# Kernel tuning notes

Hardware: AMD Instinct MI355X
Metric: run time of the kernel (lower is better)

The kernel has to match this reference:

```python
import jax, jax.numpy as jnp
import numpy as np

EMBED = 768
HEADS = 12
HEAD_DIM = EMBED // HEADS
B, S = 2, 2048


def setup_inputs() -> dict:
    key = jax.random.key(0)
    ks = jax.random.split(key, 5)
    scale = 1.0 / np.sqrt(EMBED)
    return {
        "x": jax.random.normal(ks[0], (B, S, EMBED), dtype=jnp.float32),
        "w_q": jax.random.normal(ks[1], (EMBED, EMBED), dtype=jnp.float32) * scale,
        "b_q": jnp.zeros((EMBED,), dtype=jnp.float32),
        "w_k": jax.random.normal(ks[2], (EMBED, EMBED), dtype=jnp.float32) * scale,
        "b_k": jnp.zeros((EMBED,), dtype=jnp.float32),
        "w_v": jax.random.normal(ks[3], (EMBED, EMBED), dtype=jnp.float32) * scale,
        "b_v": jnp.zeros((EMBED,), dtype=jnp.float32),
        "w_o": jax.random.normal(ks[4], (EMBED, EMBED), dtype=jnp.float32) * scale,
        "b_o": jnp.zeros((EMBED,), dtype=jnp.float32),
    }


def reference(x, w_q, b_q, w_k, b_k, w_v, b_v, w_o, b_o):
    b, s, _ = x.shape
    # QKV projections (torch Linear: y = x @ W^T + b)
    q = x @ w_q.T + b_q
    k = x @ w_k.T + b_k
    v = x @ w_v.T + b_v
    # split heads -> [b, h, s, d]
    def split(t):
        return t.reshape(b, s, HEADS, HEAD_DIM).transpose(0, 2, 1, 3)
    q, k, v = split(q), split(k), split(v)
    scores = jnp.einsum("bhqd,bhkd->bhqk", q, k) / jnp.sqrt(
        jnp.asarray(HEAD_DIM, dtype=jnp.float32))
    probs = jax.nn.softmax(scores, axis=-1)
    out = jnp.einsum("bhqk,bhkd->bhqd", probs, v)
    out = out.transpose(0, 2, 1, 3).reshape(b, s, EMBED)
    return out @ w_o.T + b_o
```

## Files before the change

### kernel.cpp

```cpp
#include <hip/hip_runtime.h>
#include <math.h>

#define EMBED 768
#define HEADS 12
#define HDIM 64
#define BATCH 2
#define SEQ 2048
#define MTOT (BATCH*SEQ)

typedef short s8v __attribute__((ext_vector_type(8)));
typedef short s4v __attribute__((ext_vector_type(4)));
typedef float f4v __attribute__((ext_vector_type(4)));

__device__ __forceinline__ short f2bf(float f) {
    union { float f; unsigned u; } v; v.f = f;
    unsigned r = v.u + 0x7FFFu + ((v.u >> 16) & 1u);
    return (short)(r >> 16);
}

__device__ __forceinline__ unsigned pkbf(float a, float b) {
#if __has_builtin(__builtin_amdgcn_cvt_pk_bf16_f32)
    typedef __bf16 b2 __attribute__((ext_vector_type(2)));
    b2 r = __builtin_amdgcn_cvt_pk_bf16_f32(a, b);
    return *(unsigned*)&r;
#else
    union { float f; unsigned u; } x, y; x.f = a; y.f = b;
    return ((y.u + 0x8000u) & 0xFFFF0000u) | ((x.u + 0x8000u) >> 16);
#endif
}

__device__ __forceinline__ float fexp2(float x) {
#if __has_builtin(__builtin_amdgcn_exp2f)
    return __builtin_amdgcn_exp2f(x);
#else
    return exp2f(x);
#endif
}

__device__ __forceinline__ void gll16(const short* g, short* l) {
    __builtin_amdgcn_global_load_lds((const __attribute__((address_space(1))) void*)g,
                                     (__attribute__((address_space(3))) void*)l, 16, 0, 0);
}

__global__ __launch_bounds__(256) void cvt_all(
        const float* __restrict__ x,  const float* __restrict__ wq,
        const float* __restrict__ wk, const float* __restrict__ wv,
        const float* __restrict__ wo,
        short* __restrict__ xb, short* __restrict__ wqb, short* __restrict__ wkb,
        short* __restrict__ wvb, short* __restrict__ wob) {
    const int seg = blockIdx.y;
    const float* src; short* dst; int n4;
    if      (seg == 0) { src = x;  dst = xb;  n4 = MTOT * EMBED / 4; }
    else if (seg == 1) { src = wq; dst = wqb; n4 = EMBED * EMBED / 4; }
    else if (seg == 2) { src = wk; dst = wkb; n4 = EMBED * EMBED / 4; }
    else if (seg == 3) { src = wv; dst = wvb; n4 = EMBED * EMBED / 4; }
    else               { src = wo; dst = wob; n4 = EMBED * EMBED / 4; }
    for (int i = blockIdx.x * 256 + threadIdx.x; i < n4; i += gridDim.x * 256) {
        float4 f = ((const float4*)src)[i];
        short4 o;
        o.x = f2bf(f.x); o.y = f2bf(f.y); o.z = f2bf(f.z); o.w = f2bf(f.w);
        ((short4*)dst)[i] = o;
    }
}

__global__ __launch_bounds__(256, 4) void gemm_qkv(const short* __restrict__ A,
        const short* __restrict__ Wq, const short* __restrict__ Wk, const short* __restrict__ Wv,
        const float* __restrict__ bq, const float* __restrict__ bk, const float* __restrict__ bv,
        short* __restrict__ Qo, short* __restrict__ Ko, short* __restrict__ Vo) {
    const int mode = blockIdx.z;
    const short* W    = (mode == 0) ? Wq : (mode == 1) ? Wk : Wv;
    const float* bias = (mode == 0) ? bq : (mode == 1) ? bk : bv;

    __shared__ short smem[12288];
    short* As0 = smem;        short* As1 = smem + 2048;
    short* Ws0 = smem + 4096; short* Ws1 = smem + 8192;

    const int tid = threadIdx.x;
    const int lane = tid & 63, wid = tid >> 6;
    const int quad = lane >> 4, lr = lane & 15;
    const int m0 = blockIdx.x * 64, n0 = blockIdx.y * 128;
    const int wm = (wid >> 1) * 32, wn = (wid & 1) * 64;
    const int ar = lane >> 2, ac = (lane & 3) * 8;

    f4v acc[2][4];
    for (int a = 0; a < 2; a++)
        for (int b = 0; b < 4; b++)
            for (int i = 0; i < 4; i++) acc[a][b][i] = 0.f;

    const short* gA  = &A[(long)(m0 + wid * 16 + ar) * EMBED + ac];
    const short* gW0 = &W[(long)(n0 + wid * 32 + ar) * EMBED + ac];
    const short* gW1 = &W[(long)(n0 + wid * 32 + 16 + ar) * EMBED + ac];
    short* dA  = smem + wid * 512;
    short* dW0 = smem + 4096 + wid * 1024;
    short* dW1 = dW0 + 512;

    gll16(gA, dA); gll16(gW0, dW0); gll16(gW1, dW1);
    gA += 32; gW0 += 32; gW1 += 32;
    __syncthreads();

    for (int k = 0; k < 24; k += 2) {
        gll16(gA, dA + 2048); gll16(gW0, dW0 + 4096); gll16(gW1, dW1 + 4096);
        gA += 32; gW0 += 32; gW1 += 32;
        {
            s8v af[2], bf[4];
            for (int mi = 0; mi < 2; mi++)
                af[mi] = *(const s8v*)&As0[(wm + mi * 16 + lr) * 32 + quad * 8];
            for (int ni = 0; ni < 4; ni++)
                bf[ni] = *(const s8v*)&Ws0[(wn + ni * 16 + lr) * 32 + quad * 8];
            for (int mi = 0; mi < 2; mi++)
                for (int ni = 0; ni < 4; ni++)
                    acc[mi][ni] = __builtin_amdgcn_mfma_f32_16x16x32_bf16(af[mi], bf[ni], acc[mi][ni], 0, 0, 0);
        }
        __syncthreads();
        if (k + 2 < 24) {
            gll16(gA, dA); gll16(gW0, dW0); gll16(gW1, dW1);
            gA += 32; gW0 += 32; gW1 += 32;
        }
        {
            s8v af[2], bf[4];
            for (int mi = 0; mi < 2; mi++)
                af[mi] = *(const s8v*)&As1[(wm + mi * 16 + lr) * 32 + quad * 8];
            for (int ni = 0; ni < 4; ni++)
                bf[ni] = *(const s8v*)&Ws1[(wn + ni * 16 + lr) * 32 + quad * 8];
            for (int mi = 0; mi < 2; mi++)
                for (int ni = 0; ni < 4; ni++)
                    acc[mi][ni] = __builtin_amdgcn_mfma_f32_16x16x32_bf16(af[mi], bf[ni], acc[mi][ni], 0, 0, 0);
        }
        __syncthreads();
    }

    float bb[4];
    for (int ni = 0; ni < 4; ni++) bb[ni] = bias[n0 + wn + ni * 16 + lr];

    if (mode == 2) {
        for (int mi = 0; mi < 2; mi++) {
            int srow = m0 + wm + mi * 16 + quad * 4;
            int b = srow >> 11, s = srow & 2047;
            int v = s & 127, r = s >> 7;
            int keyp = r * 128 + (((v >> 5) * 4 + ((v >> 2) & 3)) << 3) + ((v >> 4) & 1) * 4;
            for (int ni = 0; ni < 4; ni++) {
                int n = n0 + wn + ni * 16 + lr;
                int h = n >> 6, d = n & 63;
                uint2 pk;
                pk.x = pkbf(acc[mi][ni][0] + bb[ni], acc[mi][ni][1] + bb[ni]);
                pk.y = pkbf(acc[mi][ni][2] + bb[ni], acc[mi][ni][3] + bb[ni]);
                *(uint2*)&Vo[(((long)(b * HEADS + h) * HDIM + d) * SEQ) + keyp] = pk;
            }
        }
    } else {
        const float qsc = (mode == 0) ? 0.18033688f : 1.0f;
        short* Cs = smem;
        for (int mi = 0; mi < 2; mi++)
            for (int ni = 0; ni < 4; ni++)
                for (int i = 0; i < 4; i++)
                    Cs[(wm + mi * 16 + quad * 4 + i) * 136 + wn + ni * 16 + lr] =
                        f2bf((acc[mi][ni][i] + bb[ni]) * qsc);
        __syncthreads();
        short* Out = (mode == 0) ? Qo : Ko;
        int r = tid >> 2, seg = tid & 3;
        int m = m0 + r, b = m >> 11, s = m & 2047;
        int nn = seg * 32;
        int h = (n0 + nn) >> 6, d = nn & 63;
        short* dst = &Out[(((long)(b * HEADS + h) * SEQ + s) * HDIM) + d];
        const short* src = &Cs[r * 136 + nn];
        for (int j = 0; j < 4; j++)
            *(s8v*)(dst + j * 8) = *(const s8v*)(src + j * 8);
    }
}

__global__ __launch_bounds__(256, 4) void gemm_out(const short* __restrict__ A,
        const short* __restrict__ W, const float* __restrict__ bias,
        float* __restrict__ Out) {
    __shared__ short smem[8192];
    short* As0 = smem;        short* As1 = smem + 2048;
    short* Ws0 = smem + 4096; short* Ws1 = smem + 6144;

    const int tid = threadIdx.x;
    const int lane = tid & 63, wid = tid >> 6;
    const int quad = lane >> 4, lr = lane & 15;
    const int m0 = blockIdx.x * 64, n0 = blockIdx.y * 64;
    const int wm = (wid >> 1) * 32, wn = (wid & 1) * 32;
    const int ar = lane >> 2, ac = (lane & 3) * 8;

    f4v acc[2][2];
    for (int a = 0; a < 2; a++)
        for (int b = 0; b < 2; b++)
            for (int i = 0; i < 4; i++) acc[a][b][i] = 0.f;

    const short* gA = &A[(long)(m0 + wid * 16 + ar) * EMBED + ac];
    const short* gW = &W[(long)(n0 + wid * 16 + ar) * EMBED + ac];
    short* dA = smem + wid * 512;
    short* dW = smem + 4096 + wid * 512;

    gll16(gA, dA); gll16(gW, dW);
    gA += 32; gW += 32;
    __syncthreads();

    for (int k = 0; k < 24; k += 2) {
        gll16(gA, dA + 2048); gll16(gW, dW + 2048);
        gA += 32; gW += 32;
        {
            s8v af[2], bf[2];
            for (int mi = 0; mi < 2; mi++)
                af[mi] = *(const s8v*)&As0[(wm + mi * 16 + lr) * 32 + quad * 8];
            for (int ni = 0; ni < 2; ni++)
                bf[ni] = *(const s8v*)&Ws0[(wn + ni * 16 + lr) * 32 + quad * 8];
            for (int mi = 0; mi < 2; mi++)
                for (int ni = 0; ni < 2; ni++)
                    acc[mi][ni] = __builtin_amdgcn_mfma_f32_16x16x32_bf16(af[mi], bf[ni], acc[mi][ni], 0, 0, 0);
        }
        __syncthreads();
        if (k + 2 < 24) {
            gll16(gA, dA); gll16(gW, dW);
            gA += 32; gW += 32;
        }
        {
            s8v af[2], bf[2];
            for (int mi = 0; mi < 2; mi++)
                af[mi] = *(const s8v*)&As1[(wm + mi * 16 + lr) * 32 + quad * 8];
            for (int ni = 0; ni < 2; ni++)
                bf[ni] = *(const s8v*)&Ws1[(wn + ni * 16 + lr) * 32 + quad * 8];
            for (int mi = 0; mi < 2; mi++)
                for (int ni = 0; ni < 2; ni++)
                    acc[mi][ni] = __builtin_amdgcn_mfma_f32_16x16x32_bf16(af[mi], bf[ni], acc[mi][ni], 0, 0, 0);
        }
        __syncthreads();
    }

    for (int mi = 0; mi < 2; mi++)
        for (int ni = 0; ni < 2; ni++)
            for (int i = 0; i < 4; i++) {
                int m = m0 + wm + mi * 16 + quad * 4 + i;
                int n = n0 + wn + ni * 16 + lr;
                Out[(long)m * EMBED + n] = acc[mi][ni][i] + bias[n];
            }
}

#define VBUF (64*128)
__global__ __launch_bounds__(512, 4) void flash_attn(const short* __restrict__ Q,
        const short* __restrict__ K, const short* __restrict__ Vt,
        short* __restrict__ Out) {
    extern __shared__ char pool[];
    short* Vs = (short*)pool;
    float* Bm = (float*)pool;
    __shared__ float Ls[2][2][32];

    const int bh = blockIdx.y;
    const int tid = threadIdx.x, lane = tid & 63, wid = tid >> 6;
    const int quad = lane >> 4, lr = lane & 15;
    const int qh = wid & 1;
    const int t = wid >> 1;
    const int q0 = blockIdx.x * 64;

    const short* Qb = Q  + (long)bh * SEQ * HDIM;
    const short* Kb = K  + (long)bh * SEQ * HDIM;
    const short* Vb = Vt + (long)bh * HDIM * SEQ;

    s8v qf[2][2];
    for (int mq = 0; mq < 2; mq++)
        for (int hh = 0; hh < 2; hh++)
            qf[mq][hh] = *(const s8v*)&Qb[(q0 + qh * 32 + mq * 16 + lr) * HDIM + hh * 32 + quad * 8];

    f4v o[2][4];
    for (int mq = 0; mq < 2; mq++)
        for (int dt = 0; dt < 4; dt++)
            for (int i = 0; i < 4; i++) o[mq][dt][i] = 0.f;
    float lsum[2] = {0.f, 0.f};

    const short* kga[2];
    for (int h2 = 0; h2 < 2; h2++)
        kga[h2] = &Kb[(long)(t * 32 + h2 * 16 + lr) * HDIM + quad * 8];

    const int vrow = lane >> 4, vc = lane & 15;
    const int vd0 = wid * 8 + vrow, vd1 = wid * 8 + 4 + vrow;
    const short* vg0 = &Vb[(long)vd0 * SEQ + ((vc ^ (vd0 & 15)) * 8)];
    const short* vg1 = &Vb[(long)vd1 * SEQ + ((vc ^ (vd1 & 15)) * 8)];
    const int vsoff0 = (wid * 8) * 128, vsoff1 = (wid * 8 + 4) * 128;

    int voff[4];
    for (int dt = 0; dt < 4; dt++) {
        int d = dt * 16 + lr;
        voff[dt] = d * 128 + (((t * 4 + quad) ^ lr) * 8);
    }

    s8v kf0[4], kf1[4];

    for (int h2 = 0; h2 < 2; h2++) {
        kf0[h2 * 2]     = *(const s8v*)(kga[h2]);
        kf0[h2 * 2 + 1] = *(const s8v*)(kga[h2] + 32);
        kga[h2] += 128 * HDIM;
    }
    gll16(vg0, Vs + vsoff0); gll16(vg1, Vs + vsoff1);
    vg0 += 128; vg1 += 128;
    __syncthreads();

#define FLASH_BODY(KCUR, KNXT, CUROFF, NXTOFF, PREFETCH)                              \
    {                                                                                 \
        if (PREFETCH) {                                                               \
            for (int h2 = 0; h2 < 2; h2++) {                                          \
                KNXT[h2 * 2]     = *(const s8v*)(kga[h2]);                            \
                KNXT[h2 * 2 + 1] = *(const s8v*)(kga[h2] + 32);                       \
                kga[h2] += 128 * HDIM;                                                \
            }                                                                         \
            gll16(vg0, Vs + (NXTOFF) + vsoff0); gll16(vg1, Vs + (NXTOFF) + vsoff1);   \
            vg0 += 128; vg1 += 128;                                                   \
        }                                                                             \
        unsigned pw[2][4];                                                            \
        for (int h2 = 0; h2 < 2; h2++) {                                              \
            for (int mq = 0; mq < 2; mq++) {                                          \
                f4v s = {0.f, 0.f, 0.f, 0.f};                                         \
                s = __builtin_amdgcn_mfma_f32_16x16x32_bf16(KCUR[h2 * 2], qf[mq][0], s, 0, 0, 0); \
                s = __builtin_amdgcn_mfma_f32_16x16x32_bf16(KCUR[h2 * 2 + 1], qf[mq][1], s, 0, 0, 0); \
                float p0 = fexp2(s[0]);                                               \
                float p1 = fexp2(s[1]);                                               \
                float p2 = fexp2(s[2]);                                               \
                float p3 = fexp2(s[3]);                                               \
                lsum[mq] += (p0 + p1) + (p2 + p3);                                    \
                pw[mq][h2 * 2]     = pkbf(p0, p1);                                    \
                pw[mq][h2 * 2 + 1] = pkbf(p2, p3);                                    \
            }                                                                         \
        }                                                                             \
        s8v pf0 = *(s8v*)&pw[0][0];                                                   \
        s8v pf1 = *(s8v*)&pw[1][0];                                                   \
        for (int dt = 0; dt < 4; dt++) {                                              \
            s8v vf = *(const s8v*)&Vs[(CUROFF) + voff[dt]];                           \
            o[0][dt] = __builtin_amdgcn_mfma_f32_16x16x32_bf16(pf0, vf, o[0][dt], 0, 0, 0); \
            o[1][dt] = __builtin_amdgcn_mfma_f32_16x16x32_bf16(pf1, vf, o[1][dt], 0, 0, 0); \
        }                                                                             \
        __syncthreads();                                                              \
    }

    for (int r = 0; r < 16; r += 2) {
        FLASH_BODY(kf0, kf1, 0, VBUF, 1)
        FLASH_BODY(kf1, kf0, VBUF, 0, (r + 2 < 16))
    }
#undef FLASH_BODY

    for (int mq = 0; mq < 2; mq++) {
        lsum[mq] += __shfl_xor(lsum[mq], 16);
        lsum[mq] += __shfl_xor(lsum[mq], 32);
    }

    if (t >= 2) {
        int js = t - 2;
        for (int mq = 0; mq < 2; mq++) {
            for (int dt = 0; dt < 4; dt++)
                for (int i = 0; i < 4; i++)
                    Bm[((qh * 2 + js) * 32 + mq * 16 + quad * 4 + i) * 68 + dt * 16 + lr] = o[mq][dt][i];
            if (quad == 0) Ls[qh][js][mq * 16 + lr] = lsum[mq];
        }
    }
    __syncthreads();
    if (t < 2) {
        for (int mq = 0; mq < 2; mq++) {
            for (int dt = 0; dt < 4; dt++)
                for (int i = 0; i < 4; i++)
                    o[mq][dt][i] += Bm[((qh * 2 + t) * 32 + mq * 16 + quad * 4 + i) * 68 + dt * 16 + lr];
            lsum[mq] += Ls[qh][t][mq * 16 + lr];
        }
    }
    __syncthreads();
    if (t == 1) {
        for (int mq = 0; mq < 2; mq++) {
            for (int dt = 0; dt < 4; dt++)
                for (int i = 0; i < 4; i++)
                    Bm[((qh * 2) * 32 + mq * 16 + quad * 4 + i) * 68 + dt * 16 + lr] = o[mq][dt][i];
            if (quad == 0) Ls[qh][0][mq * 16 + lr] = lsum[mq];
        }
    }
    __syncthreads();
    if (t == 0) {
        for (int mq = 0; mq < 2; mq++) {
            for (int dt = 0; dt < 4; dt++)
                for (int i = 0; i < 4; i++)
                    o[mq][dt][i] += Bm[((qh * 2) * 32 + mq * 16 + quad * 4 + i) * 68 + dt * 16 + lr];
            lsum[mq] += Ls[qh][0][mq * 16 + lr];
            if (quad == 0) Ls[qh][0][mq * 16 + lr] = lsum[mq];
        }
    }
    __syncthreads();
    if (t == 0) {
        const int b = bh / HEADS, h = bh % HEADS;
        for (int mq = 0; mq < 2; mq++) {
            float linv[4];
            for (int i = 0; i < 4; i++)
                linv[i] = 1.0f / Ls[qh][0][mq * 16 + quad * 4 + i];
            for (int dt = 0; dt < 4; dt++) {
                for (int i = 0; i < 4; i++) {
                    int q = q0 + qh * 32 + mq * 16 + quad * 4 + i;
                    float val = o[mq][dt][i] * linv[i];
                    Out[((long)(b * SEQ + q)) * EMBED + h * HDIM + dt * 16 + lr] = f2bf(val);
                }
            }
        }
    }
}

extern "C" void kernel_launch(void* const* d_in, const int* in_sizes, int n_in,
                              void* d_out, int out_size, void* d_ws, size_t ws_size,
                              hipStream_t stream) {
    const float* x   = (const float*)d_in[0];
    const float* w_q = (const float*)d_in[1];
    const float* b_q = (const float*)d_in[2];
    const float* w_k = (const float*)d_in[3];
    const float* b_k = (const float*)d_in[4];
    const float* w_v = (const float*)d_in[5];
    const float* b_v = (const float*)d_in[6];
    const float* w_o = (const float*)d_in[7];
    const float* b_o = (const float*)d_in[8];

    short* x_bf   = (short*)d_ws;
    short* wq_bf  = x_bf  + MTOT * EMBED;
    short* wk_bf  = wq_bf + EMBED * EMBED;
    short* wv_bf  = wk_bf + EMBED * EMBED;
    short* wo_bf  = wv_bf + EMBED * EMBED;
    short* q_bf   = wo_bf + EMBED * EMBED;
    short* k_bf   = q_bf  + BATCH * HEADS * SEQ * HDIM;
    short* v_bf   = k_bf  + BATCH * HEADS * SEQ * HDIM;
    short* att_bf = v_bf  + BATCH * HEADS * SEQ * HDIM;

    cvt_all<<<dim3(1024, 5), 256, 0, stream>>>(x, w_q, w_k, w_v, w_o,
                                               x_bf, wq_bf, wk_bf, wv_bf, wo_bf);

    gemm_qkv<<<dim3(MTOT / 64, EMBED / 128, 3), 256, 0, stream>>>(
        x_bf, wq_bf, wk_bf, wv_bf, b_q, b_k, b_v, q_bf, k_bf, v_bf);

    flash_attn<<<dim3(SEQ / 64, BATCH * HEADS), 512, 34816, stream>>>(
        q_bf, k_bf, v_bf, att_bf);

    gemm_out<<<dim3(MTOT / 64, EMBED / 64), 256, 0, stream>>>(
        att_bf, wo_bf, b_o, (float*)d_out);
}
```

Before: 186.5 us.

## Stage K tiles in double-buffered swizzled LDS via async global-to-LDS loads

The attention kernel no longer loads K fragments straight from global memory into registers in every wave. K tiles are now copied into double-buffered, XOR-swizzled shared memory with asynchronous global-to-LDS loads, the same way V is already handled, and waves read their fragments from LDS. This removes the duplicate global K reads across waves and frees the registers that held prefetched K. In exchange, dynamic shared memory per block grows to 64KB, which may lower how many blocks fit on a CU.

Measured after the change: 194.2 us. 1.04x slower.

```diff
diff --git a/kernel.cpp b/kernel.cpp
--- a/kernel.cpp
+++ b/kernel.cpp
@@ -236,14 +236,18 @@
             }
 }
 
+#define KBUF (128*64)
 #define VBUF (64*128)
 __global__ __launch_bounds__(512, 4) void flash_attn(const short* __restrict__ Q,
         const short* __restrict__ K, const short* __restrict__ Vt,
         short* __restrict__ Out) {
     extern __shared__ char pool[];
-    short* Vs = (short*)pool;
-    float* Bm = (float*)pool;
-    __shared__ float Ls[2][2][32];
+    short* Ks0 = (short*)pool;
+    short* Ks1 = Ks0 + KBUF;
+    short* Vs0 = Ks1 + KBUF;
+    short* Vs1 = Vs0 + VBUF;
+    float* Bm  = (float*)pool;
+    float* Ls  = (float*)(pool + 34816);
 
     const int bh = blockIdx.y;
     const int tid = threadIdx.x, lane = tid & 63, wid = tid >> 6;
@@ -267,50 +271,51 @@
             for (int i = 0; i < 4; i++) o[mq][dt][i] = 0.f;
     float lsum[2] = {0.f, 0.f};
 
-    const short* kga[2];
-    for (int h2 = 0; h2 < 2; h2++)
-        kga[h2] = &Kb[(long)(t * 32 + h2 * 16 + lr) * HDIM + quad * 8];
-
+    const int krow = lane >> 3, kc = lane & 7;
+    const int kgc = ((kc ^ krow) & 7) * 8;
+    const int ksoff0 = (wid * 16) * 64, ksoff1 = (wid * 16 + 8) * 64;
+    const short* kg0 = &Kb[(long)(wid * 16 + krow) * HDIM + kgc];
+    const short* kg1 = &Kb[(long)(wid * 16 + 8 + krow) * HDIM + kgc];
     const int vrow = lane >> 4, vc = lane & 15;
     const int vd0 = wid * 8 + vrow, vd1 = wid * 8 + 4 + vrow;
+    const int vsoff0 = (wid * 8) * 128, vsoff1 = (wid * 8 + 4) * 128;
     const short* vg0 = &Vb[(long)vd0 * SEQ + ((vc ^ (vd0 & 15)) * 8)];
     const short* vg1 = &Vb[(long)vd1 * SEQ + ((vc ^ (vd1 & 15)) * 8)];
-    const int vsoff0 = (wid * 8) * 128, vsoff1 = (wid * 8 + 4) * 128;
-
+
+    int kao[2], ka1o[2];
+    for (int h2 = 0; h2 < 2; h2++) {
+        int row = t * 32 + h2 * 16 + lr;
+        kao[h2]  = row * 64 + ((quad ^ (lr & 7)) * 8);
+        ka1o[h2] = row * 64 + (((4 + quad) ^ (lr & 7)) * 8);
+    }
     int voff[4];
     for (int dt = 0; dt < 4; dt++) {
         int d = dt * 16 + lr;
         voff[dt] = d * 128 + (((t * 4 + quad) ^ lr) * 8);
     }
 
-    s8v kf0[4], kf1[4];
-
-    for (int h2 = 0; h2 < 2; h2++) {
-        kf0[h2 * 2]     = *(const s8v*)(kga[h2]);
-        kf0[h2 * 2 + 1] = *(const s8v*)(kga[h2] + 32);
-        kga[h2] += 128 * HDIM;
-    }
-    gll16(vg0, Vs + vsoff0); gll16(vg1, Vs + vsoff1);
+    gll16(kg0, Ks0 + ksoff0); gll16(kg1, Ks0 + ksoff1);
+    gll16(vg0, Vs0 + vsoff0); gll16(vg1, Vs0 + vsoff1);
+    kg0 += 128 * HDIM; kg1 += 128 * HDIM;
     vg0 += 128; vg1 += 128;
     __syncthreads();
 
-#define FLASH_BODY(KCUR, KNXT, CUROFF, NXTOFF, PREFETCH)                              \
+#define FLASH_BODY(KCUR, VCUR, KNXT, VNXT, PREFETCH)                                  \
     {                                                                                 \
         if (PREFETCH) {                                                               \
-            for (int h2 = 0; h2 < 2; h2++) {                                          \
-                KNXT[h2 * 2]     = *(const s8v*)(kga[h2]);                            \
-                KNXT[h2 * 2 + 1] = *(const s8v*)(kga[h2] + 32);                       \
-                kga[h2] += 128 * HDIM;                                                \
-            }                                                                         \
-            gll16(vg0, Vs + (NXTOFF) + vsoff0); gll16(vg1, Vs + (NXTOFF) + vsoff1);   \
+            gll16(kg0, (KNXT) + ksoff0); gll16(kg1, (KNXT) + ksoff1);                 \
+            gll16(vg0, (VNXT) + vsoff0); gll16(vg1, (VNXT) + vsoff1);                 \
+            kg0 += 128 * HDIM; kg1 += 128 * HDIM;                                     \
             vg0 += 128; vg1 += 128;                                                   \
         }                                                                             \
         unsigned pw[2][4];                                                            \
         for (int h2 = 0; h2 < 2; h2++) {                                              \
+            s8v kf0 = *(const s8v*)((KCUR) + kao[h2]);                                \
+            s8v kf1 = *(const s8v*)((KCUR) + ka1o[h2]);                               \
             for (int mq = 0; mq < 2; mq++) {                                          \
                 f4v s = {0.f, 0.f, 0.f, 0.f};                                         \
-                s = __builtin_amdgcn_mfma_f32_16x16x32_bf16(KCUR[h2 * 2], qf[mq][0], s, 0, 0, 0); \
-                s = __builtin_amdgcn_mfma_f32_16x16x32_bf16(KCUR[h2 * 2 + 1], qf[mq][1], s, 0, 0, 0); \
+                s = __builtin_amdgcn_mfma_f32_16x16x32_bf16(kf0, qf[mq][0], s, 0, 0, 0); \
+                s = __builtin_amdgcn_mfma_f32_16x16x32_bf16(kf1, qf[mq][1], s, 0, 0, 0); \
                 float p0 = fexp2(s[0]);                                               \
                 float p1 = fexp2(s[1]);                                               \
                 float p2 = fexp2(s[2]);                                               \
@@ -323,7 +328,7 @@
         s8v pf0 = *(s8v*)&pw[0][0];                                                   \
         s8v pf1 = *(s8v*)&pw[1][0];                                                   \
         for (int dt = 0; dt < 4; dt++) {                                              \
-            s8v vf = *(const s8v*)&Vs[(CUROFF) + voff[dt]];                           \
+            s8v vf = *(const s8v*)((VCUR) + voff[dt]);                                \
             o[0][dt] = __builtin_amdgcn_mfma_f32_16x16x32_bf16(pf0, vf, o[0][dt], 0, 0, 0); \
             o[1][dt] = __builtin_amdgcn_mfma_f32_16x16x32_bf16(pf1, vf, o[1][dt], 0, 0, 0); \
         }                                                                             \
@@ -331,8 +336,8 @@
     }
 
     for (int r = 0; r < 16; r += 2) {
-        FLASH_BODY(kf0, kf1, 0, VBUF, 1)
-        FLASH_BODY(kf1, kf0, VBUF, 0, (r + 2 < 16))
+        FLASH_BODY(Ks0, Vs0, Ks1, Vs1, 1)
+        FLASH_BODY(Ks1, Vs1, Ks0, Vs0, (r + 2 < 16))
     }
 #undef FLASH_BODY
 
@@ -347,7 +352,7 @@
             for (int dt = 0; dt < 4; dt++)
                 for (int i = 0; i < 4; i++)
                     Bm[((qh * 2 + js) * 32 + mq * 16 + quad * 4 + i) * 68 + dt * 16 + lr] = o[mq][dt][i];
-            if (quad == 0) Ls[qh][js][mq * 16 + lr] = lsum[mq];
+            if (quad == 0) Ls[(qh * 2 + js) * 32 + mq * 16 + lr] = lsum[mq];
         }
     }
     __syncthreads();
@@ -356,7 +361,7 @@
             for (int dt = 0; dt < 4; dt++)
                 for (int i = 0; i < 4; i++)
                     o[mq][dt][i] += Bm[((qh * 2 + t) * 32 + mq * 16 + quad * 4 + i) * 68 + dt * 16 + lr];
-            lsum[mq] += Ls[qh][t][mq * 16 + lr];
+            lsum[mq] += Ls[(qh * 2 + t) * 32 + mq * 16 + lr];
         }
     }
     __syncthreads();
@@ -365,7 +370,7 @@
             for (int dt = 0; dt < 4; dt++)
                 for (int i = 0; i < 4; i++)
                     Bm[((qh * 2) * 32 + mq * 16 + quad * 4 + i) * 68 + dt * 16 + lr] = o[mq][dt][i];
-            if (quad == 0) Ls[qh][0][mq * 16 + lr] = lsum[mq];
+            if (quad == 0) Ls[(qh * 2) * 32 + mq * 16 + lr] = lsum[mq];
         }
     }
     __syncthreads();
@@ -374,8 +379,8 @@
             for (int dt = 0; dt < 4; dt++)
                 for (int i = 0; i < 4; i++)
                     o[mq][dt][i] += Bm[((qh * 2) * 32 + mq * 16 + quad * 4 + i) * 68 + dt * 16 + lr];
-            lsum[mq] += Ls[qh][0][mq * 16 + lr];
-            if (quad == 0) Ls[qh][0][mq * 16 + lr] = lsum[mq];
+            lsum[mq] += Ls[(qh * 2) * 32 + mq * 16 + lr];
+            if (quad == 0) Ls[(qh * 2) * 32 + mq * 16 + lr] = lsum[mq];
         }
     }
     __syncthreads();
@@ -384,7 +389,7 @@
         for (int mq = 0; mq < 2; mq++) {
             float linv[4];
             for (int i = 0; i < 4; i++)
-                linv[i] = 1.0f / Ls[qh][0][mq * 16 + quad * 4 + i];
+                linv[i] = 1.0f / Ls[(qh * 2) * 32 + mq * 16 + quad * 4 + i];
             for (int dt = 0; dt < 4; dt++) {
                 for (int i = 0; i < 4; i++) {
                     int q = q0 + qh * 32 + mq * 16 + quad * 4 + i;
@@ -425,7 +430,7 @@
     gemm_qkv<<<dim3(MTOT / 64, EMBED / 128, 3), 256, 0, stream>>>(
         x_bf, wq_bf, wk_bf, wv_bf, b_q, b_k, b_v, q_bf, k_bf, v_bf);
 
-    flash_attn<<<dim3(SEQ / 64, BATCH * HEADS), 512, 34816, stream>>>(
+    flash_attn<<<dim3(SEQ / 64, BATCH * HEADS), 512, 65536, stream>>>(
         q_bf, k_bf, v_bf, att_bf);
 
     gemm_out<<<dim3(MTOT / 64, EMBED / 64), 256, 0, stream>>>(
```
